# Kernel optimization log

Measured on AMD Instinct MI355X. Metric: run time of the kernel, lower is better.

The kernel has to match this reference:

```python
import jax, jax.numpy as jnp
import numpy as np

EPS = 1e-5  # torch BatchNorm default eps
SLOPE = 0.2  # LeakyReLU negative slope


def bn_apply(h, p):
    # p: (4, C) stacked [gamma, beta, running_mean, running_var]; h channel-last
    g, b, m, v = p[0], p[1], p[2], p[3]
    return (h - m) * (g * jax.lax.rsqrt(v + EPS)) + b


def graph_feature(x, k):
    # x: (B, N, C) -> (B, N, k, 2C) = concat(neighbor - center, center)
    inner = jnp.einsum('bnc,bmc->bnm', x, x)
    sq = jnp.sum(x * x, axis=-1)
    # negative squared pairwise distance (B, N, N)
    pd = 2.0 * inner - sq[:, :, None] - sq[:, None, :]
    idx = jax.lax.top_k(pd, k)[1]  # (B, N, k)
    nbr = jax.vmap(lambda xb, ib: xb[ib])(x, idx)  # (B, N, k, C) gather
    ctr = jnp.broadcast_to(x[:, :, None, :], nbr.shape)
    return jnp.concatenate([nbr - ctr, ctr], axis=-1)


def edge_block(h, w, bnp, k):
    # h: (B, N, C); w: (O, 2C) 1x1 conv weight; returns (B, N, O) after max over k
    f = graph_feature(h, k)
    z = jnp.einsum('bnkc,oc->bnko', f, w)
    z = jax.nn.leaky_relu(bn_apply(z, bnp), SLOPE)
    return jnp.max(z, axis=2)


def setup_inputs() -> dict:
    key = jax.random.key(0)
    ks = jax.random.split(key, 10)
    B, N, K = 16, 1024, 20
    emb, ncls = 1024, 40

    def bnp(c):
        return jnp.stack([jnp.ones(c), jnp.zeros(c), jnp.zeros(c), jnp.ones(c)])

    s = 0.05
    return {
        'x': jax.random.normal(ks[0], (B, 3, N), dtype=jnp.float32),
        'w1': jax.random.normal(ks[1], (64, 6), dtype=jnp.float32) * s,
        'bn1': bnp(64),
        'w2': jax.random.normal(ks[2], (64, 128), dtype=jnp.float32) * s,
        'bn2': bnp(64),
        'w3': jax.random.normal(ks[3], (128, 128), dtype=jnp.float32) * s,
        'bn3': bnp(128),
        'w4': jax.random.normal(ks[4], (256, 256), dtype=jnp.float32) * s,
        'bn4': bnp(256),
        'w5': jax.random.normal(ks[5], (emb, 512), dtype=jnp.float32) * s,
        'bn5': bnp(emb),
        'wl1': jax.random.normal(ks[6], (512, 2 * emb), dtype=jnp.float32) * s,
        'bn6': bnp(512),
        'wl2': jax.random.normal(ks[7], (256, 512), dtype=jnp.float32) * s,
        'bn7': bnp(256),
        'wl3': jax.random.normal(ks[8], (ncls, 256), dtype=jnp.float32) * s,
        'bl3': jax.random.normal(ks[9], (ncls,), dtype=jnp.float32) * s,
        'k': K,
    }


def reference(x, w1, bn1, w2, bn2, w3, bn3, w4, bn4, w5, bn5,
              wl1, bn6, wl2, bn7, wl3, bl3, k):
    # x: (B, 3, N) -> logits (B, num_classes); eval-mode BN, dropout = identity
    h0 = jnp.transpose(x, (0, 2, 1))  # (B, N, 3)
    x1 = edge_block(h0, w1, bn1, k)   # (B, N, 64)
    x2 = edge_block(x1, w2, bn2, k)   # (B, N, 64)
    x3 = edge_block(x2, w3, bn3, k)   # (B, N, 128)
    x4 = edge_block(x3, w4, bn4, k)   # (B, N, 256)
    h = jnp.concatenate([x1, x2, x3, x4], axis=-1)  # (B, N, 512)
    h = jax.nn.leaky_relu(bn_apply(jnp.einsum('bnc,oc->bno', h, w5), bn5), SLOPE)
    p = jnp.concatenate([jnp.max(h, axis=1), jnp.mean(h, axis=1)], axis=-1)  # (B, 2*emb)
    h = jax.nn.leaky_relu(bn_apply(p @ wl1.T, bn6), SLOPE)
    h = jax.nn.leaky_relu(bn_apply(h @ wl2.T, bn7), SLOPE)
    return h @ wl3.T + bl3
```

## Files before the change

### kernel.cpp

```cpp
#include <hip/hip_runtime.h>

#define BB 16
#define NN 1024
#define KNN 20
#define BNEPS 1e-5f

typedef __attribute__((ext_vector_type(8))) short short8;
typedef __attribute__((ext_vector_type(4))) float f32x4;

__device__ __forceinline__ float4 ld4(const float* p){ return *(const float4*)p; }
__device__ __forceinline__ void fma4(float4& a, float s, float4 w){
  a.x = fmaf(s, w.x, a.x); a.y = fmaf(s, w.y, a.y);
  a.z = fmaf(s, w.z, a.z); a.w = fmaf(s, w.w, a.w);
}
__device__ __forceinline__ void max4(float4& a, float4 v){
  a.x = fmaxf(a.x, v.x); a.y = fmaxf(a.y, v.y);
  a.z = fmaxf(a.z, v.z); a.w = fmaxf(a.w, v.w);
}
__device__ __forceinline__ unsigned short f2bf(float f){
  unsigned int u = __float_as_uint(f);
  u = (u + 0x7FFF + ((u >> 16) & 1)) >> 16;
  return (unsigned short)u;
}
__device__ __forceinline__ float bf2f(unsigned short u){
  return __uint_as_float(((unsigned int)u) << 16);
}
__device__ __forceinline__ f32x4 mfma16(short8 a, short8 b, f32x4 c){
  return __builtin_amdgcn_mfma_f32_16x16x32_bf16(a, b, c, 0, 0, 0);
}

__device__ __forceinline__ void top3_build(const float* rp, int kmr,
                                           float& a0, float& a1, float& a2,
                                           int& i0, int& i1, int& i2){
  a0 = -1e30f; a1 = -1e30f; a2 = -1e30f; i0 = 0; i1 = 0; i2 = 0;
#pragma unroll
  for (int r = 0; r < 4; r++){
    float4 t = ld4(rp + r*4);
    float tv[4] = {t.x, t.y, t.z, t.w};
#pragma unroll
    for (int q = 0; q < 4; q++){
      int e = r*4 + q;
      float v = ((kmr >> e) & 1) ? -1e30f : tv[q];
      bool b0 = v > a0, b1 = v > a1, b2 = v > a2;
      a2 = b1 ? a1 : (b2 ? v : a2); i2 = b1 ? i1 : (b2 ? e : i2);
      a1 = b0 ? a0 : (b1 ? v : a1); i1 = b0 ? i0 : (b1 ? e : i1);
      a0 = b0 ? v  : a0;            i0 = b0 ? e : i0;
    }
  }
}

__global__ __launch_bounds__(256) void k_transpose(const float* __restrict__ x, float* __restrict__ xt,
                                                   unsigned short* __restrict__ hlo,
                                                   float* __restrict__ sq){
  int i = blockIdx.x*256 + threadIdx.x;
  if (i >= BB*NN) return;
  int b = i >> 10, n = i & 1023;
  const float* xb = x + (size_t)b*3*NN;
  float4 v;
  v.x = xb[0*NN+n]; v.y = xb[1*NN+n]; v.z = xb[2*NN+n]; v.w = 0.f;
  ((float4*)xt)[i] = v;
  unsigned short hx = f2bf(v.x), hy = f2bf(v.y), hz = f2bf(v.z);
  float rx = v.x - bf2f(hx), ry = v.y - bf2f(hy), rz = v.z - bf2f(hz);
  unsigned short lx = f2bf(rx), ly = f2bf(ry), lz = f2bf(rz);
  float ex = bf2f(hx)+bf2f(lx), ey = bf2f(hy)+bf2f(ly), ez = bf2f(hz)+bf2f(lz);
  sq[i] = ex*ex + ey*ey + ez*ez;
  ushort4 h4 = {hx, hy, hz, 0};
  ushort4 l4 = {lx, ly, lz, 0};
  ushort4 z4 = {0, 0, 0, 0};
  unsigned short* pa = hlo + (size_t)i*512 + 256;
  unsigned short* pb = hlo + (size_t)i*512 + 288;
  *(ushort4*)(pa+0) = h4; *(ushort4*)(pa+4) = l4; *(ushort4*)(pa+8) = h4;
  *(ushort4*)(pb+0) = h4; *(ushort4*)(pb+4) = h4; *(ushort4*)(pb+8) = l4;
#pragma unroll
  for (int s = 12; s < 32; s += 4){ *(ushort4*)(pa+s) = z4; *(ushort4*)(pb+s) = z4; }
}

__device__ __forceinline__ void prep_w_dev(int i, const float* w, const float* bnp,
                                           float* wlT, float* dT, float* bias, int Cin, int Cpad, int Cout){
  if (i >= Cpad*Cout) return;
  int c = i / Cout, o = i - c*Cout;
  float s = bnp[o] * rsqrtf(bnp[3*Cout+o] + BNEPS);
  float wl = (c < Cin) ? w[(size_t)o*2*Cin + c] : 0.f;
  float wr = (c < Cin) ? w[(size_t)o*2*Cin + Cin + c] : 0.f;
  wlT[i] = wl * s;
  dT[i]  = (wr - wl) * s;
  if (c == 0) bias[o] = bnp[Cout+o] - bnp[2*Cout+o]*s;
}
__device__ __forceinline__ void prep_wbf_dev(int i, const float* w, const float* bnp,
                                             unsigned short* wlB, unsigned short* dB, float* bias,
                                             int Cin, int Cout){
  if (i >= Cin*Cout) return;
  int o = i / Cin, c = i - o*Cin;
  float s = bnp[o] * rsqrtf(bnp[3*Cout+o] + BNEPS);
  float wl = w[(size_t)o*2*Cin + c] * s;
  float wr = w[(size_t)o*2*Cin + Cin + c] * s;
  wlB[i] = f2bf(wl);
  dB[i]  = f2bf(wr - wl);
  if (c == 0) bias[o] = bnp[Cout+o] - bnp[2*Cout+o]*s;
}

__global__ __launch_bounds__(256) void k_prep_all(const float* __restrict__ w1, const float* __restrict__ bn1,
                                                  const float* __restrict__ w2, const float* __restrict__ bn2,
                                                  const float* __restrict__ w3, const float* __restrict__ bn3,
                                                  const float* __restrict__ w4, const float* __restrict__ bn4,
                                                  const float* __restrict__ w5, const float* __restrict__ bn5,
                                                  float* __restrict__ wlT1, float* __restrict__ dT1, float* __restrict__ bias1,
                                                  unsigned short* __restrict__ wlB2, unsigned short* __restrict__ dB2, float* __restrict__ bias2,
                                                  unsigned short* __restrict__ wlB3, unsigned short* __restrict__ dB3, float* __restrict__ bias3,
                                                  unsigned short* __restrict__ wlB4, unsigned short* __restrict__ dB4, float* __restrict__ bias4,
                                                  unsigned short* __restrict__ w5b, float* __restrict__ b5){
  int bid = blockIdx.x, t = threadIdx.x;
  if (bid < 1){
    prep_w_dev(t, w1, bn1, wlT1, dT1, bias1, 3, 4, 64);
  } else if (bid < 17){
    prep_wbf_dev((bid-1)*256 + t, w2, bn2, wlB2, dB2, bias2, 64, 64);
  } else if (bid < 49){
    prep_wbf_dev((bid-17)*256 + t, w3, bn3, wlB3, dB3, bias3, 64, 128);
  } else if (bid < 177){
    prep_wbf_dev((bid-49)*256 + t, w4, bn4, wlB4, dB4, bias4, 128, 256);
  } else {
    int i = (bid-177)*256 + t;
    int o = i >> 9, c = i & 511;
    float s = bn5[o] * rsqrtf(bn5[3*1024+o] + BNEPS);
    w5b[i] = f2bf(w5[(size_t)o*512 + c] * s);
    if (c == 0) b5[o] = bn5[1024+o] - bn5[2*1024+o]*s;
  }
}

template<int CC>
__global__ __launch_bounds__(256) void k_pdm(const unsigned short* __restrict__ hbi,
                                             const unsigned short* __restrict__ hlo,
                                             const float* __restrict__ sq,
                                             float* __restrict__ pd){
  __shared__ char sm[20480];
  char* As = sm; char* Bs = sm + 10240;
  const int tid = threadIdx.x, lane = tid & 63, w = tid >> 6;
  const int l15 = lane & 15, quad = lane >> 4;
  const int bid = blockIdx.x;
  const int xcd = bid & 7, j = bid >> 3;
  const int b = xcd + ((j >> 6) << 3);
  const int rt = (j >> 3) & 7, ct = j & 7;
  const size_t ar0 = (size_t)b*NN + rt*128;
  const size_t br0 = (size_t)b*NN + ct*128;
  const int colb = ct*128;

  f32x4 acc[2][8];
  f32x4 zero = {0.f,0.f,0.f,0.f};
#pragma unroll
  for (int i = 0; i < 2; i++)
#pragma unroll
    for (int j2 = 0; j2 < 8; j2++) acc[i][j2] = zero;

  for (int k0 = 0; k0 < 3*CC; k0 += 32){
    int seg = k0 / CC, off = k0 - seg*CC;
    const unsigned short* Ap = (seg == 1) ? hlo : hbi;
    const unsigned short* Bp = (seg == 2) ? hlo : hbi;
#pragma unroll
    for (int i = 0; i < 2; i++){
      int e = tid + i*256;
      int r = e >> 2, sg = e & 3;
      *(float4*)(As + r*80 + sg*16) = *(const float4*)(Ap + (ar0+r)*512 + off + sg*8);
      *(float4*)(Bs + r*80 + sg*16) = *(const float4*)(Bp + (br0+r)*512 + off + sg*8);
    }
    __syncthreads();
    short8 af0 = *(short8*)(As + (w*32 + l15)*80 + quad*16);
    short8 af1 = *(short8*)(As + (w*32 + 16 + l15)*80 + quad*16);
#pragma unroll
    for (int ns = 0; ns < 8; ns++){
      short8 bf = *(short8*)(Bs + (ns*16 + l15)*80 + quad*16);
      acc[0][ns] = mfma16(af0, bf, acc[0][ns]);
      acc[1][ns] = mfma16(af1, bf, acc[1][ns]);
    }
    __syncthreads();
  }

  float* L = (float*)sm;
#pragma unroll
  for (int p = 0; p < 4; p++){
    const int ms = p >> 1, nh = p & 1;
    __syncthreads();
#pragma unroll
    for (int ns = 0; ns < 4; ns++){
      f32x4 a = acc[ms][nh*4 + ns];
      float sqv = sq[br0 + (nh*4+ns)*16 + l15];
#pragma unroll
      for (int r = 0; r < 4; r++)
        L[(w*16 + quad*4 + r)*68 + ns*16 + l15] = 2.f*a[r] - sqv;
    }
    __syncthreads();
#pragma unroll
    for (int k = 0; k < 4; k++){
      int e = tid + k*256;
      int lr = e >> 4, c4 = (e & 15)*4;
      int grow = (int)ar0 + (lr >> 4)*32 + ms*16 + (lr & 15);
      *(float4*)(pd + (size_t)grow*NN + colb + nh*64 + c4) = *(float4*)(L + lr*68 + c4);
    }
  }
}

__global__ __launch_bounds__(256) void k_pdm1(const unsigned short* __restrict__ hlo,
                                              const float* __restrict__ sq,
                                              float* __restrict__ pd){
  __shared__ char sm[20480];
  char* As = sm; char* Bs = sm + 10240;
  const int tid = threadIdx.x, lane = tid & 63, w = tid >> 6;
  const int l15 = lane & 15, quad = lane >> 4;
  const int bid = blockIdx.x;
  const int xcd = bid & 7, j = bid >> 3;
  const int b = xcd + ((j >> 6) << 3);
  const int rt = (j >> 3) & 7, ct = j & 7;
  const size_t ar0 = (size_t)b*NN + rt*128;
  const size_t br0 = (size_t)b*NN + ct*128;
  const int colb = ct*128;

#pragma unroll
  for (int i = 0; i < 2; i++){
    int e = tid + i*256;
    int r = e >> 2, sg = e & 3;
    *(float4*)(As + r*80 + sg*16) = *(const float4*)(hlo + (ar0+r)*512 + 256 + sg*8);
    *(float4*)(Bs + r*80 + sg*16) = *(const float4*)(hlo + (br0+r)*512 + 288 + sg*8);
  }
  __syncthreads();

  f32x4 acc[2][8];
  f32x4 zero = {0.f,0.f,0.f,0.f};
#pragma unroll
  for (int i = 0; i < 2; i++)
#pragma unroll
    for (int j2 = 0; j2 < 8; j2++) acc[i][j2] = zero;

  short8 af0 = *(short8*)(As + (w*32 + l15)*80 + quad*16);
  short8 af1 = *(short8*)(As + (w*32 + 16 + l15)*80 + quad*16);
#pragma unroll
  for (int ns = 0; ns < 8; ns++){
    short8 bf = *(short8*)(Bs + (ns*16 + l15)*80 + quad*16);
    acc[0][ns] = mfma16(af0, bf, acc[0][ns]);
    acc[1][ns] = mfma16(af1, bf, acc[1][ns]);
  }

  float* L = (float*)sm;
#pragma unroll
  for (int p = 0; p < 4; p++){
    const int ms = p >> 1, nh = p & 1;
    __syncthreads();
#pragma unroll
    for (int ns = 0; ns < 4; ns++){
      f32x4 a = acc[ms][nh*4 + ns];
      float sqv = sq[br0 + (nh*4+ns)*16 + l15];
#pragma unroll
      for (int r = 0; r < 4; r++)
        L[(w*16 + quad*4 + r)*68 + ns*16 + l15] = 2.f*a[r] - sqv;
    }
    __syncthreads();
#pragma unroll
    for (int k = 0; k < 4; k++){
      int e = tid + k*256;
      int lr = e >> 4, c4 = (e & 15)*4;
      int grow = (int)ar0 + (lr >> 4)*32 + ms*16 + (lr & 15);
      *(float4*)(pd + (size_t)grow*NN + colb + nh*64 + c4) = *(float4*)(L + lr*68 + c4);
    }
  }
}

__global__ __launch_bounds__(256) void k_topk(const float* __restrict__ pd, int* __restrict__ idxOut){
  int w = threadIdx.x >> 6, lane = threadIdx.x & 63;
  const int bid = blockIdx.x;
  const int xcd = bid & 7, j = bid >> 3;
  const int b = xcd + ((j >> 7) << 3);
  const int local = j & 127;
  int bn0 = (b*128 + local)*8 + w*2;
  const float* row0 = pd + (size_t)bn0*NN + lane*16;
  const float* row1 = row0 + NN;

  float c0v[2], c1v[2], c2v[2];
  int   c0i[2], c1i[2], c2i[2];
  int   km[2] = {0, 0};
  top3_build(row0, 0, c0v[0], c1v[0], c2v[0], c0i[0], c1i[0], c2i[0]);
  top3_build(row1, 0, c0v[1], c1v[1], c2v[1], c0i[1], c1i[1], c2i[1]);

  int* out0 = idxOut + (size_t)bn0*KNN;
  int* out1 = out0 + KNN;
  for (int it = 0; it < KNN; it++){
    float g0 = c0v[0], g1 = c0v[1];
#pragma unroll
    for (int s = 1; s < 64; s <<= 1){
      g0 = fmaxf(g0, __shfl_xor(g0, s));
      g1 = fmaxf(g1, __shfl_xor(g1, s));
    }
    int o0 = __ffsll(__ballot(c0v[0] == g0)) - 1;
    int o1 = __ffsll(__ballot(c0v[1] == g1)) - 1;
    bool u0 = (lane == o0), u1 = (lane == o1);
    if (u0) out0[it] = lane*16 + c0i[0];
    if (u1) out1[it] = lane*16 + c0i[1];
    km[0] |= u0 ? (1 << c0i[0]) : 0;
    km[1] |= u1 ? (1 << c0i[1]) : 0;
    c0v[0] = u0 ? c1v[0] : c0v[0];  c0i[0] = u0 ? c1i[0] : c0i[0];
    c1v[0] = u0 ? c2v[0] : c1v[0];  c1i[0] = u0 ? c2i[0] : c1i[0];
    c2v[0] = u0 ? -1e30f : c2v[0];
    c0v[1] = u1 ? c1v[1] : c0v[1];  c0i[1] = u1 ? c1i[1] : c0i[1];
    c1v[1] = u1 ? c2v[1] : c1v[1];  c1i[1] = u1 ? c2i[1] : c1i[1];
    c2v[1] = u1 ? -1e30f : c2v[1];
    if (it < KNN-1){
      bool rp0 = (c0v[0] == -1e30f) && (km[0] != 0xFFFF);
      bool rp1 = (c0v[1] == -1e30f) && (km[1] != 0xFFFF);
      if (__ballot(rp0 || rp1)){
        if (rp0) top3_build(row0, km[0], c0v[0], c1v[0], c2v[0], c0i[0], c1i[0], c2i[0]);
        if (rp1) top3_build(row1, km[1], c0v[1], c1v[1], c2v[1], c0i[1], c1i[1], c2i[1]);
      }
    }
  }
}

__global__ __launch_bounds__(256) void k_uv1(const float* __restrict__ xt,
                                             const float* __restrict__ wlT, const float* __restrict__ dT,
                                             float* __restrict__ Z){
  const int bid = blockIdx.x;
  const int pb = ((bid >> 10) << 10) | ((bid & 7) << 7) | ((bid >> 3) & 127);
  int t = pb*256 + threadIdx.x;
  int n = t >> 5, q = t & 31;
  float4 xv = ld4(xt + (size_t)n*4);
  const float* wp = (q < 16) ? (wlT + q*4) : (dT + (q-16)*4);
  float4 a = make_float4(0.f,0.f,0.f,0.f);
  fma4(a, xv.x, ld4(wp + 0*64));
  fma4(a, xv.y, ld4(wp + 1*64));
  fma4(a, xv.z, ld4(wp + 2*64));
  fma4(a, xv.w, ld4(wp + 3*64));
  *(float4*)(Z + (size_t)n*128 + q*4) = a;
}

template<int K>
__global__ __launch_bounds__(256) void k_uv(const unsigned short* __restrict__ hbi,
                                            const unsigned short* __restrict__ wB,
                                            float* __restrict__ Z, int ldz){
  __shared__ char sm[20480];
  char* As = sm; char* Bs = sm + 10240;
  const int tid = threadIdx.x, lane = tid & 63, w = tid >> 6;
  const int l15 = lane & 15, quad = lane >> 4;
  const int bx = blockIdx.x;
  const int t = ((bx & 7) << 3) | ((bx >> 3) & 7) | (bx & 64);
  const int n0 = blockIdx.y*128, r0 = t*128;

  f32x4 acc[2][8];
  f32x4 zero = {0.f,0.f,0.f,0.f};
#pragma unroll
  for (int i = 0; i < 2; i++)
#pragma unroll
    for (int j = 0; j < 8; j++) acc[i][j] = zero;

  for (int k0 = 0; k0 < K; k0 += 32){
#pragma unroll
    for (int i = 0; i < 2; i++){
      int e = tid + i*256;
      int r = e >> 2, sg = e & 3;
      *(float4*)(As + r*80 + sg*16) = *(const float4*)(hbi + ((size_t)(r0+r))*512 + k0 + sg*8);
      *(float4*)(Bs + r*80 + sg*16) = *(const float4*)(wB  + ((size_t)(n0+r))*K   + k0 + sg*8);
    }
    __syncthreads();
    short8 af0 = *(short8*)(As + (w*32 + l15)*80 + quad*16);
    short8 af1 = *(short8*)(As + (w*32 + 16 + l15)*80 + quad*16);
#pragma unroll
    for (int ns = 0; ns < 8; ns++){
      short8 bf = *(short8*)(Bs + (ns*16 + l15)*80 + quad*16);
      acc[0][ns] = mfma16(af0, bf, acc[0][ns]);
      acc[1][ns] = mfma16(af1, bf, acc[1][ns]);
    }
    __syncthreads();
  }

#pragma unroll
  for (int ms = 0; ms < 2; ms++){
#pragma unroll
    for (int ns = 0; ns < 8; ns++){
      f32x4 a = acc[ms][ns];
      int row = r0 + w*32 + ms*16 + quad*4;
      int col = n0 + ns*16 + l15;
#pragma unroll
      for (int r = 0; r < 4; r++)
        Z[(size_t)(row+r)*ldz + col] = a[r];
    }
  }
}

template<int COUT, int P, bool WLO>
__global__ __launch_bounds__(256) void k_gmax(const float* __restrict__ Z,
                                              const float* __restrict__ bias,
                                              const int* __restrict__ knn_idx,
                                              unsigned short* __restrict__ hbo,
                                              unsigned short* __restrict__ hloo,
                                              float* __restrict__ sqo){
  constexpr int QPP = COUT/4;
  constexpr int BPB = 1024/P;
  constexpr int SHF = (P == 16) ? 6 : (P == 8) ? 7 : 8;
  __shared__ int idxS[P*KNN];
  const int tid = threadIdx.x;
  const int bid = blockIdx.x;
  const int pb = ((bid >> (SHF+3)) << (SHF+3)) | ((bid & 7) << SHF) | ((bid >> 3) & (BPB-1));
  const int p0 = pb * P;
  for (int t = tid; t < P*KNN; t += 256) idxS[t] = knn_idx[(size_t)p0*KNN + t];
  __syncthreads();

  const int p = tid / QPP, q = tid - p*QPP;
  const int base = p0 & ~1023;
  const int ldz = 2*COUT;
  const float* Zq = Z + q*4;

  float4 m = make_float4(-1e30f,-1e30f,-1e30f,-1e30f);
#pragma unroll
  for (int j = 0; j < KNN; j++){
    int mr = idxS[p*KNN + j];
    max4(m, ld4(Zq + (size_t)(base + mr)*ldz));
  }
  float4 ctr = ld4(Z + (size_t)(p0+p)*ldz + COUT + q*4);
  float4 bs  = ld4(bias + q*4);
  float4 y;
  y.x = m.x + ctr.x + bs.x; y.x = fmaxf(y.x, 0.2f*y.x);
  y.y = m.y + ctr.y + bs.y; y.y = fmaxf(y.y, 0.2f*y.y);
  y.z = m.z + ctr.z + bs.z; y.z = fmaxf(y.z, 0.2f*y.z);
  y.w = m.w + ctr.w + bs.w; y.w = fmaxf(y.w, 0.2f*y.w);

  size_t pi = (size_t)(p0 + p);
  ushort4 hv; hv.x = f2bf(y.x); hv.y = f2bf(y.y); hv.z = f2bf(y.z); hv.w = f2bf(y.w);
  *(ushort4*)(hbo + pi*512 + q*4) = hv;
  if (WLO){
    ushort4 lv;
    lv.x = f2bf(y.x - bf2f(hv.x)); lv.y = f2bf(y.y - bf2f(hv.y));
    lv.z = f2bf(y.z - bf2f(hv.z)); lv.w = f2bf(y.w - bf2f(hv.w));
    *(ushort4*)(hloo + pi*512 + q*4) = lv;
    float ex = bf2f(hv.x)+bf2f(lv.x), ey = bf2f(hv.y)+bf2f(lv.y);
    float ez = bf2f(hv.z)+bf2f(lv.z), ew = bf2f(hv.w)+bf2f(lv.w);
    float s4 = ex*ex + ey*ey + ez*ez + ew*ew;
#pragma unroll
    for (int sh = 1; sh < QPP; sh <<= 1) s4 += __shfl_xor(s4, sh);
    if (q == 0) sqo[pi] = s4;
  }
}

__global__ __launch_bounds__(256) void k_conv5m(const unsigned short* __restrict__ hb,
                                                const unsigned short* __restrict__ w5b,
                                                const float* __restrict__ b5,
                                                float* __restrict__ pmax, float* __restrict__ psum){
  __shared__ char sm[20480 + 4096];
  char* As = sm; char* Bs = sm + 10240;
  float* red = (float*)(sm + 20480);
  const int tid = threadIdx.x, lane = tid & 63, w = tid >> 6;
  const int l15 = lane & 15, quad = lane >> 4;
  const int n0 = blockIdx.y*128, r0 = blockIdx.x*128;

  f32x4 acc[2][8];
  f32x4 zero = {0.f,0.f,0.f,0.f};
#pragma unroll
  for (int i = 0; i < 2; i++)
#pragma unroll
    for (int j = 0; j < 8; j++) acc[i][j] = zero;

  for (int k0 = 0; k0 < 512; k0 += 32){
#pragma unroll
    for (int i = 0; i < 2; i++){
      int e = tid + i*256;
      int r = e >> 2, sg = e & 3;
      *(float4*)(As + r*80 + sg*16) = *(const float4*)(hb  + ((size_t)(r0+r))*512 + k0 + sg*8);
      *(float4*)(Bs + r*80 + sg*16) = *(const float4*)(w5b + ((size_t)(n0+r))*512 + k0 + sg*8);
    }
    __syncthreads();
    short8 af0 = *(short8*)(As + (w*32 + l15)*80 + quad*16);
    short8 af1 = *(short8*)(As + (w*32 + 16 + l15)*80 + quad*16);
#pragma unroll
    for (int ns = 0; ns < 8; ns++){
      short8 bf = *(short8*)(Bs + (ns*16 + l15)*80 + quad*16);
      acc[0][ns] = mfma16(af0, bf, acc[0][ns]);
      acc[1][ns] = mfma16(af1, bf, acc[1][ns]);
    }
    __syncthreads();
  }

#pragma unroll
  for (int ns = 0; ns < 8; ns++){
    float bv = b5[n0 + ns*16 + l15];
    float mx = -1e30f, sum = 0.f;
#pragma unroll
    for (int ms = 0; ms < 2; ms++){
      float* a = (float*)&acc[ms][ns];
#pragma unroll
      for (int r = 0; r < 4; r++){
        float v = a[r] + bv; v = fmaxf(v, 0.2f*v);
        mx = fmaxf(mx, v); sum += v;
      }
    }
    for (int s = 16; s < 64; s <<= 1){
      mx = fmaxf(mx, __shfl_xor(mx, s));
      sum += __shfl_xor(sum, s);
    }
    if (quad == 0){ red[(w*8 + ns)*16 + l15] = mx; red[512 + (w*8 + ns)*16 + l15] = sum; }
  }
  __syncthreads();
  if (tid < 128){
    int ns = tid >> 4, ci = tid & 15;
    float mx = -1e30f, sum = 0.f;
#pragma unroll
    for (int w2 = 0; w2 < 4; w2++){
      mx = fmaxf(mx, red[(w2*8 + ns)*16 + ci]);
      sum += red[512 + (w2*8 + ns)*16 + ci];
    }
    pmax[(size_t)blockIdx.x*1024 + n0 + tid] = mx;
    psum[(size_t)blockIdx.x*1024 + n0 + tid] = sum;
  }
}

__global__ __launch_bounds__(256) void k_fc1(const float* __restrict__ pmax, const float* __restrict__ psum,
                                             const float* __restrict__ wl1, const float* __restrict__ bn6,
                                             float* __restrict__ h1){
  __shared__ float pS[2048];
  const int b = blockIdx.y, t = threadIdx.x;
  for (int f = t; f < 512; f += 256){
    float4 r;
    if (f < 256){
      r = ld4(pmax + (size_t)(b*8)*1024 + f*4);
#pragma unroll
      for (int ch = 1; ch < 8; ch++) max4(r, ld4(pmax + (size_t)(b*8+ch)*1024 + f*4));
    } else {
      int o = (f-256)*4;
      r = ld4(psum + (size_t)(b*8)*1024 + o);
#pragma unroll
      for (int ch = 1; ch < 8; ch++){
        float4 s = ld4(psum + (size_t)(b*8+ch)*1024 + o);
        r.x += s.x; r.y += s.y; r.z += s.z; r.w += s.w;
      }
      r.x *= (1.f/1024.f); r.y *= (1.f/1024.f); r.z *= (1.f/1024.f); r.w *= (1.f/1024.f);
    }
    ((float4*)pS)[f] = r;
  }
  __syncthreads();
  const int ol = t >> 4, ch = t & 15;
  const int o = blockIdx.x*16 + ol;
  const float* wr = wl1 + (size_t)o*2048;
  float acc = 0.f;
#pragma unroll
  for (int j = 0; j < 32; j++){
    int c = ch*4 + j*64;
    float4 wv = ld4(wr + c);
    acc += pS[c]*wv.x + pS[c+1]*wv.y + pS[c+2]*wv.z + pS[c+3]*wv.w;
  }
#pragma unroll
  for (int s = 1; s < 16; s <<= 1) acc += __shfl_xor(acc, s);
  if (ch == 0){
    float s = bn6[o] * rsqrtf(bn6[3*512+o] + BNEPS);
    float y = (acc - bn6[2*512+o])*s + bn6[512+o];
    h1[(size_t)b*512 + o] = fmaxf(y, 0.2f*y);
  }
}

__global__ __launch_bounds__(256) void k_fc2(const float* __restrict__ h1,
                                             const float* __restrict__ wl2, const float* __restrict__ bn7,
                                             float* __restrict__ h2){
  __shared__ float hS[512];
  const int b = blockIdx.y, t = threadIdx.x;
  if (t < 128) ((float4*)hS)[t] = ((const float4*)(h1 + (size_t)b*512))[t];
  __syncthreads();
  const int ol = t >> 4, ch = t & 15;
  const int o = blockIdx.x*16 + ol;
  const float* wr = wl2 + (size_t)o*512;
  float acc = 0.f;
#pragma unroll
  for (int j = 0; j < 8; j++){
    int c = ch*4 + j*64;
    float4 wv = ld4(wr + c);
    acc += hS[c]*wv.x + hS[c+1]*wv.y + hS[c+2]*wv.z + hS[c+3]*wv.w;
  }
#pragma unroll
  for (int s = 1; s < 16; s <<= 1) acc += __shfl_xor(acc, s);
  if (ch == 0){
    float s = bn7[o] * rsqrtf(bn7[3*256+o] + BNEPS);
    float y = (acc - bn7[2*256+o])*s + bn7[256+o];
    h2[(size_t)b*256 + o] = fmaxf(y, 0.2f*y);
  }
}

__global__ __launch_bounds__(64) void k_fc3(const float* __restrict__ h2,
                                            const float* __restrict__ wl3, const float* __restrict__ bl3,
                                            float* __restrict__ out){
  const int o = blockIdx.x, b = blockIdx.y, lane = threadIdx.x;
  float4 wv = ld4(wl3 + (size_t)o*256 + lane*4);
  float4 hv = ld4(h2 + (size_t)b*256 + lane*4);
  float acc = hv.x*wv.x + hv.y*wv.y + hv.z*wv.z + hv.w*wv.w;
#pragma unroll
  for (int s = 1; s < 64; s <<= 1) acc += __shfl_xor(acc, s);
  if (lane == 0) out[(size_t)b*40 + o] = acc + bl3[o];
}

extern "C" void kernel_launch(void* const* d_in, const int* in_sizes, int n_in,
                              void* d_out, int out_size, void* d_ws, size_t ws_size,
                              hipStream_t stream) {
  (void)in_sizes; (void)n_in; (void)out_size; (void)ws_size;
  const float* x   = (const float*)d_in[0];
  const float* w1  = (const float*)d_in[1];
  const float* bn1 = (const float*)d_in[2];
  const float* w2  = (const float*)d_in[3];
  const float* bn2 = (const float*)d_in[4];
  const float* w3  = (const float*)d_in[5];
  const float* bn3 = (const float*)d_in[6];
  const float* w4  = (const float*)d_in[7];
  const float* bn4 = (const float*)d_in[8];
  const float* w5  = (const float*)d_in[9];
  const float* bn5 = (const float*)d_in[10];
  const float* wl1 = (const float*)d_in[11];
  const float* bn6 = (const float*)d_in[12];
  const float* wl2 = (const float*)d_in[13];
  const float* bn7 = (const float*)d_in[14];
  const float* wl3 = (const float*)d_in[15];
  const float* bl3 = (const float*)d_in[16];
  float* out = (float*)d_out;

  float* ws    = (float*)d_ws;
  float* xt    = ws;
  float* sqb   = xt + 65536;
  int*   idxb  = (int*)(sqb + 16384);
  float* pd    = (float*)(idxb + 327680);
  unsigned short* hlo = (unsigned short*)(pd + 16777216);
  float* wlT1  = (float*)(hlo + 8388608);
  float* dT1   = wlT1 + 256;
  float* bias1 = dT1 + 256;
  float* bias2 = bias1 + 64;
  float* bias3 = bias2 + 64;
  float* bias4 = bias3 + 128;
  float* b5    = bias4 + 256;
  float* pmax  = b5 + 1024;
  float* psum  = pmax + 131072;
  float* pool  = psum + 131072;
  float* h1b   = pool + 32768;
  float* h2b   = h1b + 8192;
  unsigned short* hb   = (unsigned short*)(h2b + 4096);
  unsigned short* wlB2 = hb + (size_t)16384*512;
  unsigned short* dB2  = wlB2 + 4096;
  unsigned short* wlB3 = dB2 + 4096;
  unsigned short* dB3  = wlB3 + 8192;
  unsigned short* wlB4 = dB3 + 8192;
  unsigned short* dB4  = wlB4 + 32768;
  unsigned short* w5b  = dB4 + 32768;
  float* Z = pd;

  k_transpose<<<64, 256, 0, stream>>>(x, xt, hlo, sqb);
  k_prep_all<<<2225, 256, 0, stream>>>(w1, bn1, w2, bn2, w3, bn3, w4, bn4, w5, bn5,
                                       wlT1, dT1, bias1, wlB2, dB2, bias2,
                                       wlB3, dB3, bias3, wlB4, dB4, bias4, w5b, b5);

  k_pdm1<<<1024, 256, 0, stream>>>(hlo, sqb, pd);
  k_topk<<<2048, 256, 0, stream>>>(pd, idxb);
  k_uv1<<<2048, 256, 0, stream>>>(xt, wlT1, dT1, Z);
  k_gmax<64,16,true><<<1024, 256, 0, stream>>>(Z, bias1, idxb, hb, hlo, sqb);

  k_pdm<64><<<1024, 256, 0, stream>>>(hb, hlo, sqb, pd);
  k_topk<<<2048, 256, 0, stream>>>(pd, idxb);
  k_uv<64><<<dim3(128,1), 256, 0, stream>>>(hb, wlB2, Z, 128);
  k_gmax<64,16,true><<<1024, 256, 0, stream>>>(Z, bias2, idxb, hb + 64, hlo + 64, sqb);

  k_pdm<64><<<1024, 256, 0, stream>>>(hb + 64, hlo + 64, sqb, pd);
  k_topk<<<2048, 256, 0, stream>>>(pd, idxb);
  k_uv<64><<<dim3(128,2), 256, 0, stream>>>(hb + 64, wlB3, Z, 256);
  k_gmax<128,8,true><<<2048, 256, 0, stream>>>(Z, bias3, idxb, hb + 128, hlo + 128, sqb);

  k_pdm<128><<<1024, 256, 0, stream>>>(hb + 128, hlo + 128, sqb, pd);
  k_topk<<<2048, 256, 0, stream>>>(pd, idxb);
  k_uv<128><<<dim3(128,4), 256, 0, stream>>>(hb + 128, wlB4, Z, 512);
  k_gmax<256,4,false><<<4096, 256, 0, stream>>>(Z, bias4, idxb, hb + 256, nullptr, nullptr);

  k_conv5m<<<dim3(128,8), 256, 0, stream>>>(hb, w5b, b5, pmax, psum);
  k_fc1<<<dim3(32,16), 256, 0, stream>>>(pmax, psum, wl1, bn6, h1b);
  k_fc2<<<dim3(16,16), 256, 0, stream>>>(h1b, wl2, bn7, h2b);
  k_fc3<<<dim3(40,16), 64, 0, stream>>>(h2b, wl3, bl3, out);
}
```

Before: 422.1 us.

## Co-launch top-k with per-point projection GEMM and merge init kernels

Runs top-k selection and the per-point weight projection GEMM in one launch, with blocks split by index range. Z gets its own buffer, so the two no longer alias pd and can run concurrently. The transpose and weight-prep kernels are also merged into one init launch. This cuts launch overhead and lets independent work overlap to fill the GPU, at the cost of a larger workspace and mixed block types sharing occupancy.

```diff
diff --git a/kernel.cpp b/kernel.cpp
--- a/kernel.cpp
+++ b/kernel.cpp
@@ -49,222 +49,9 @@
   }
 }
 
-__global__ __launch_bounds__(256) void k_transpose(const float* __restrict__ x, float* __restrict__ xt,
-                                                   unsigned short* __restrict__ hlo,
-                                                   float* __restrict__ sq){
-  int i = blockIdx.x*256 + threadIdx.x;
-  if (i >= BB*NN) return;
-  int b = i >> 10, n = i & 1023;
-  const float* xb = x + (size_t)b*3*NN;
-  float4 v;
-  v.x = xb[0*NN+n]; v.y = xb[1*NN+n]; v.z = xb[2*NN+n]; v.w = 0.f;
-  ((float4*)xt)[i] = v;
-  unsigned short hx = f2bf(v.x), hy = f2bf(v.y), hz = f2bf(v.z);
-  float rx = v.x - bf2f(hx), ry = v.y - bf2f(hy), rz = v.z - bf2f(hz);
-  unsigned short lx = f2bf(rx), ly = f2bf(ry), lz = f2bf(rz);
-  float ex = bf2f(hx)+bf2f(lx), ey = bf2f(hy)+bf2f(ly), ez = bf2f(hz)+bf2f(lz);
-  sq[i] = ex*ex + ey*ey + ez*ez;
-  ushort4 h4 = {hx, hy, hz, 0};
-  ushort4 l4 = {lx, ly, lz, 0};
-  ushort4 z4 = {0, 0, 0, 0};
-  unsigned short* pa = hlo + (size_t)i*512 + 256;
-  unsigned short* pb = hlo + (size_t)i*512 + 288;
-  *(ushort4*)(pa+0) = h4; *(ushort4*)(pa+4) = l4; *(ushort4*)(pa+8) = h4;
-  *(ushort4*)(pb+0) = h4; *(ushort4*)(pb+4) = h4; *(ushort4*)(pb+8) = l4;
-#pragma unroll
-  for (int s = 12; s < 32; s += 4){ *(ushort4*)(pa+s) = z4; *(ushort4*)(pb+s) = z4; }
-}
-
-__device__ __forceinline__ void prep_w_dev(int i, const float* w, const float* bnp,
-                                           float* wlT, float* dT, float* bias, int Cin, int Cpad, int Cout){
-  if (i >= Cpad*Cout) return;
-  int c = i / Cout, o = i - c*Cout;
-  float s = bnp[o] * rsqrtf(bnp[3*Cout+o] + BNEPS);
-  float wl = (c < Cin) ? w[(size_t)o*2*Cin + c] : 0.f;
-  float wr = (c < Cin) ? w[(size_t)o*2*Cin + Cin + c] : 0.f;
-  wlT[i] = wl * s;
-  dT[i]  = (wr - wl) * s;
-  if (c == 0) bias[o] = bnp[Cout+o] - bnp[2*Cout+o]*s;
-}
-__device__ __forceinline__ void prep_wbf_dev(int i, const float* w, const float* bnp,
-                                             unsigned short* wlB, unsigned short* dB, float* bias,
-                                             int Cin, int Cout){
-  if (i >= Cin*Cout) return;
-  int o = i / Cin, c = i - o*Cin;
-  float s = bnp[o] * rsqrtf(bnp[3*Cout+o] + BNEPS);
-  float wl = w[(size_t)o*2*Cin + c] * s;
-  float wr = w[(size_t)o*2*Cin + Cin + c] * s;
-  wlB[i] = f2bf(wl);
-  dB[i]  = f2bf(wr - wl);
-  if (c == 0) bias[o] = bnp[Cout+o] - bnp[2*Cout+o]*s;
-}
-
-__global__ __launch_bounds__(256) void k_prep_all(const float* __restrict__ w1, const float* __restrict__ bn1,
-                                                  const float* __restrict__ w2, const float* __restrict__ bn2,
-                                                  const float* __restrict__ w3, const float* __restrict__ bn3,
-                                                  const float* __restrict__ w4, const float* __restrict__ bn4,
-                                                  const float* __restrict__ w5, const float* __restrict__ bn5,
-                                                  float* __restrict__ wlT1, float* __restrict__ dT1, float* __restrict__ bias1,
-                                                  unsigned short* __restrict__ wlB2, unsigned short* __restrict__ dB2, float* __restrict__ bias2,
-                                                  unsigned short* __restrict__ wlB3, unsigned short* __restrict__ dB3, float* __restrict__ bias3,
-                                                  unsigned short* __restrict__ wlB4, unsigned short* __restrict__ dB4, float* __restrict__ bias4,
-                                                  unsigned short* __restrict__ w5b, float* __restrict__ b5){
-  int bid = blockIdx.x, t = threadIdx.x;
-  if (bid < 1){
-    prep_w_dev(t, w1, bn1, wlT1, dT1, bias1, 3, 4, 64);
-  } else if (bid < 17){
-    prep_wbf_dev((bid-1)*256 + t, w2, bn2, wlB2, dB2, bias2, 64, 64);
-  } else if (bid < 49){
-    prep_wbf_dev((bid-17)*256 + t, w3, bn3, wlB3, dB3, bias3, 64, 128);
-  } else if (bid < 177){
-    prep_wbf_dev((bid-49)*256 + t, w4, bn4, wlB4, dB4, bias4, 128, 256);
-  } else {
-    int i = (bid-177)*256 + t;
-    int o = i >> 9, c = i & 511;
-    float s = bn5[o] * rsqrtf(bn5[3*1024+o] + BNEPS);
-    w5b[i] = f2bf(w5[(size_t)o*512 + c] * s);
-    if (c == 0) b5[o] = bn5[1024+o] - bn5[2*1024+o]*s;
-  }
-}
-
-template<int CC>
-__global__ __launch_bounds__(256) void k_pdm(const unsigned short* __restrict__ hbi,
-                                             const unsigned short* __restrict__ hlo,
-                                             const float* __restrict__ sq,
-                                             float* __restrict__ pd){
-  __shared__ char sm[20480];
-  char* As = sm; char* Bs = sm + 10240;
-  const int tid = threadIdx.x, lane = tid & 63, w = tid >> 6;
-  const int l15 = lane & 15, quad = lane >> 4;
-  const int bid = blockIdx.x;
-  const int xcd = bid & 7, j = bid >> 3;
-  const int b = xcd + ((j >> 6) << 3);
-  const int rt = (j >> 3) & 7, ct = j & 7;
-  const size_t ar0 = (size_t)b*NN + rt*128;
-  const size_t br0 = (size_t)b*NN + ct*128;
-  const int colb = ct*128;
-
-  f32x4 acc[2][8];
-  f32x4 zero = {0.f,0.f,0.f,0.f};
-#pragma unroll
-  for (int i = 0; i < 2; i++)
-#pragma unroll
-    for (int j2 = 0; j2 < 8; j2++) acc[i][j2] = zero;
-
-  for (int k0 = 0; k0 < 3*CC; k0 += 32){
-    int seg = k0 / CC, off = k0 - seg*CC;
-    const unsigned short* Ap = (seg == 1) ? hlo : hbi;
-    const unsigned short* Bp = (seg == 2) ? hlo : hbi;
-#pragma unroll
-    for (int i = 0; i < 2; i++){
-      int e = tid + i*256;
-      int r = e >> 2, sg = e & 3;
-      *(float4*)(As + r*80 + sg*16) = *(const float4*)(Ap + (ar0+r)*512 + off + sg*8);
-      *(float4*)(Bs + r*80 + sg*16) = *(const float4*)(Bp + (br0+r)*512 + off + sg*8);
-    }
-    __syncthreads();
-    short8 af0 = *(short8*)(As + (w*32 + l15)*80 + quad*16);
-    short8 af1 = *(short8*)(As + (w*32 + 16 + l15)*80 + quad*16);
-#pragma unroll
-    for (int ns = 0; ns < 8; ns++){
-      short8 bf = *(short8*)(Bs + (ns*16 + l15)*80 + quad*16);
-      acc[0][ns] = mfma16(af0, bf, acc[0][ns]);
-      acc[1][ns] = mfma16(af1, bf, acc[1][ns]);
-    }
-    __syncthreads();
-  }
-
-  float* L = (float*)sm;
-#pragma unroll
-  for (int p = 0; p < 4; p++){
-    const int ms = p >> 1, nh = p & 1;
-    __syncthreads();
-#pragma unroll
-    for (int ns = 0; ns < 4; ns++){
-      f32x4 a = acc[ms][nh*4 + ns];
-      float sqv = sq[br0 + (nh*4+ns)*16 + l15];
-#pragma unroll
-      for (int r = 0; r < 4; r++)
-        L[(w*16 + quad*4 + r)*68 + ns*16 + l15] = 2.f*a[r] - sqv;
-    }
-    __syncthreads();
-#pragma unroll
-    for (int k = 0; k < 4; k++){
-      int e = tid + k*256;
-      int lr = e >> 4, c4 = (e & 15)*4;
-      int grow = (int)ar0 + (lr >> 4)*32 + ms*16 + (lr & 15);
-      *(float4*)(pd + (size_t)grow*NN + colb + nh*64 + c4) = *(float4*)(L + lr*68 + c4);
-    }
-  }
-}
-
-__global__ __launch_bounds__(256) void k_pdm1(const unsigned short* __restrict__ hlo,
-                                              const float* __restrict__ sq,
-                                              float* __restrict__ pd){
-  __shared__ char sm[20480];
-  char* As = sm; char* Bs = sm + 10240;
-  const int tid = threadIdx.x, lane = tid & 63, w = tid >> 6;
-  const int l15 = lane & 15, quad = lane >> 4;
-  const int bid = blockIdx.x;
-  const int xcd = bid & 7, j = bid >> 3;
-  const int b = xcd + ((j >> 6) << 3);
-  const int rt = (j >> 3) & 7, ct = j & 7;
-  const size_t ar0 = (size_t)b*NN + rt*128;
-  const size_t br0 = (size_t)b*NN + ct*128;
-  const int colb = ct*128;
-
-#pragma unroll
-  for (int i = 0; i < 2; i++){
-    int e = tid + i*256;
-    int r = e >> 2, sg = e & 3;
-    *(float4*)(As + r*80 + sg*16) = *(const float4*)(hlo + (ar0+r)*512 + 256 + sg*8);
-    *(float4*)(Bs + r*80 + sg*16) = *(const float4*)(hlo + (br0+r)*512 + 288 + sg*8);
-  }
-  __syncthreads();
-
-  f32x4 acc[2][8];
-  f32x4 zero = {0.f,0.f,0.f,0.f};
-#pragma unroll
-  for (int i = 0; i < 2; i++)
-#pragma unroll
-    for (int j2 = 0; j2 < 8; j2++) acc[i][j2] = zero;
-
-  short8 af0 = *(short8*)(As + (w*32 + l15)*80 + quad*16);
-  short8 af1 = *(short8*)(As + (w*32 + 16 + l15)*80 + quad*16);
-#pragma unroll
-  for (int ns = 0; ns < 8; ns++){
-    short8 bf = *(short8*)(Bs + (ns*16 + l15)*80 + quad*16);
-    acc[0][ns] = mfma16(af0, bf, acc[0][ns]);
-    acc[1][ns] = mfma16(af1, bf, acc[1][ns]);
-  }
-
-  float* L = (float*)sm;
-#pragma unroll
-  for (int p = 0; p < 4; p++){
-    const int ms = p >> 1, nh = p & 1;
-    __syncthreads();
-#pragma unroll
-    for (int ns = 0; ns < 4; ns++){
-      f32x4 a = acc[ms][nh*4 + ns];
-      float sqv = sq[br0 + (nh*4+ns)*16 + l15];
-#pragma unroll
-      for (int r = 0; r < 4; r++)
-        L[(w*16 + quad*4 + r)*68 + ns*16 + l15] = 2.f*a[r] - sqv;
-    }
-    __syncthreads();
-#pragma unroll
-    for (int k = 0; k < 4; k++){
-      int e = tid + k*256;
-      int lr = e >> 4, c4 = (e & 15)*4;
-      int grow = (int)ar0 + (lr >> 4)*32 + ms*16 + (lr & 15);
-      *(float4*)(pd + (size_t)grow*NN + colb + nh*64 + c4) = *(float4*)(L + lr*68 + c4);
-    }
-  }
-}
-
-__global__ __launch_bounds__(256) void k_topk(const float* __restrict__ pd, int* __restrict__ idxOut){
-  int w = threadIdx.x >> 6, lane = threadIdx.x & 63;
-  const int bid = blockIdx.x;
+__device__ __forceinline__ void topk_body(int bid, int tidx,
+                                          const float* __restrict__ pd, int* __restrict__ idxOut){
+  int w = tidx >> 6, lane = tidx & 63;
   const int xcd = bid & 7, j = bid >> 3;
   const int b = xcd + ((j >> 7) << 3);
   const int local = j & 127;
@@ -311,10 +98,287 @@
   }
 }
 
-__global__ __launch_bounds__(256) void k_uv1(const float* __restrict__ xt,
-                                             const float* __restrict__ wlT, const float* __restrict__ dT,
-                                             float* __restrict__ Z){
+__device__ __forceinline__ void prep_w_dev(int i, const float* w, const float* bnp,
+                                           float* wlT, float* dT, float* bias, int Cin, int Cpad, int Cout){
+  if (i >= Cpad*Cout) return;
+  int c = i / Cout, o = i - c*Cout;
+  float s = bnp[o] * rsqrtf(bnp[3*Cout+o] + BNEPS);
+  float wl = (c < Cin) ? w[(size_t)o*2*Cin + c] : 0.f;
+  float wr = (c < Cin) ? w[(size_t)o*2*Cin + Cin + c] : 0.f;
+  wlT[i] = wl * s;
+  dT[i]  = (wr - wl) * s;
+  if (c == 0) bias[o] = bnp[Cout+o] - bnp[2*Cout+o]*s;
+}
+__device__ __forceinline__ void prep_wbf_dev(int i, const float* w, const float* bnp,
+                                             unsigned short* wlB, unsigned short* dB, float* bias,
+                                             int Cin, int Cout){
+  if (i >= Cin*Cout) return;
+  int o = i / Cin, c = i - o*Cin;
+  float s = bnp[o] * rsqrtf(bnp[3*Cout+o] + BNEPS);
+  float wl = w[(size_t)o*2*Cin + c] * s;
+  float wr = w[(size_t)o*2*Cin + Cin + c] * s;
+  wlB[i] = f2bf(wl);
+  dB[i]  = f2bf(wr - wl);
+  if (c == 0) bias[o] = bnp[Cout+o] - bnp[2*Cout+o]*s;
+}
+
+__global__ __launch_bounds__(256) void k_init(const float* __restrict__ x, float* __restrict__ xt,
+                                              unsigned short* __restrict__ hlo, float* __restrict__ sq,
+                                              const float* __restrict__ w1, const float* __restrict__ bn1,
+                                              const float* __restrict__ w2, const float* __restrict__ bn2,
+                                              const float* __restrict__ w3, const float* __restrict__ bn3,
+                                              const float* __restrict__ w4, const float* __restrict__ bn4,
+                                              const float* __restrict__ w5, const float* __restrict__ bn5,
+                                              float* __restrict__ wlT1, float* __restrict__ dT1, float* __restrict__ bias1,
+                                              unsigned short* __restrict__ wlB2, unsigned short* __restrict__ dB2, float* __restrict__ bias2,
+                                              unsigned short* __restrict__ wlB3, unsigned short* __restrict__ dB3, float* __restrict__ bias3,
+                                              unsigned short* __restrict__ wlB4, unsigned short* __restrict__ dB4, float* __restrict__ bias4,
+                                              unsigned short* __restrict__ w5b, float* __restrict__ b5){
+  const int t = threadIdx.x;
+  if (blockIdx.x < 64){
+    int i = blockIdx.x*256 + t;
+    int b = i >> 10, n = i & 1023;
+    const float* xb = x + (size_t)b*3*NN;
+    float4 v;
+    v.x = xb[0*NN+n]; v.y = xb[1*NN+n]; v.z = xb[2*NN+n]; v.w = 0.f;
+    ((float4*)xt)[i] = v;
+    unsigned short hx = f2bf(v.x), hy = f2bf(v.y), hz = f2bf(v.z);
+    float rx = v.x - bf2f(hx), ry = v.y - bf2f(hy), rz = v.z - bf2f(hz);
+    unsigned short lx = f2bf(rx), ly = f2bf(ry), lz = f2bf(rz);
+    float ex = bf2f(hx)+bf2f(lx), ey = bf2f(hy)+bf2f(ly), ez = bf2f(hz)+bf2f(lz);
+    sq[i] = ex*ex + ey*ey + ez*ez;
+    ushort4 h4 = {hx, hy, hz, 0};
+    ushort4 l4 = {lx, ly, lz, 0};
+    ushort4 z4 = {0, 0, 0, 0};
+    unsigned short* pa = hlo + (size_t)i*512 + 256;
+    unsigned short* pb = hlo + (size_t)i*512 + 288;
+    *(ushort4*)(pa+0) = h4; *(ushort4*)(pa+4) = l4; *(ushort4*)(pa+8) = h4;
+    *(ushort4*)(pb+0) = h4; *(ushort4*)(pb+4) = h4; *(ushort4*)(pb+8) = l4;
+#pragma unroll
+    for (int s = 12; s < 32; s += 4){ *(ushort4*)(pa+s) = z4; *(ushort4*)(pb+s) = z4; }
+    return;
+  }
+  int bid = blockIdx.x - 64;
+  if (bid < 1){
+    prep_w_dev(t, w1, bn1, wlT1, dT1, bias1, 3, 4, 64);
+  } else if (bid < 17){
+    prep_wbf_dev((bid-1)*256 + t, w2, bn2, wlB2, dB2, bias2, 64, 64);
+  } else if (bid < 49){
+    prep_wbf_dev((bid-17)*256 + t, w3, bn3, wlB3, dB3, bias3, 64, 128);
+  } else if (bid < 177){
+    prep_wbf_dev((bid-49)*256 + t, w4, bn4, wlB4, dB4, bias4, 128, 256);
+  } else {
+    int i = (bid-177)*256 + t;
+    int o = i >> 9, c = i & 511;
+    float s = bn5[o] * rsqrtf(bn5[3*1024+o] + BNEPS);
+    w5b[i] = f2bf(w5[(size_t)o*512 + c] * s);
+    if (c == 0) b5[o] = bn5[1024+o] - bn5[2*1024+o]*s;
+  }
+}
+
+template<int CC>
+__global__ __launch_bounds__(256) void k_pdm(const unsigned short* __restrict__ hbi,
+                                             const unsigned short* __restrict__ hlo,
+                                             const float* __restrict__ sq,
+                                             float* __restrict__ pd){
+  __shared__ char sm[20480];
+  char* As = sm; char* Bs = sm + 10240;
+  const int tid = threadIdx.x, lane = tid & 63, w = tid >> 6;
+  const int l15 = lane & 15, quad = lane >> 4;
   const int bid = blockIdx.x;
+  const int xcd = bid & 7, j = bid >> 3;
+  const int b = xcd + ((j >> 6) << 3);
+  const int rt = (j >> 3) & 7, ct = j & 7;
+  const size_t ar0 = (size_t)b*NN + rt*128;
+  const size_t br0 = (size_t)b*NN + ct*128;
+  const int colb = ct*128;
+
+  f32x4 acc[2][8];
+  f32x4 zero = {0.f,0.f,0.f,0.f};
+#pragma unroll
+  for (int i = 0; i < 2; i++)
+#pragma unroll
+    for (int j2 = 0; j2 < 8; j2++) acc[i][j2] = zero;
+
+  for (int k0 = 0; k0 < 3*CC; k0 += 32){
+    int seg = k0 / CC, off = k0 - seg*CC;
+    const unsigned short* Ap = (seg == 1) ? hlo : hbi;
+    const unsigned short* Bp = (seg == 2) ? hlo : hbi;
+#pragma unroll
+    for (int i = 0; i < 2; i++){
+      int e = tid + i*256;
+      int r = e >> 2, sg = e & 3;
+      *(float4*)(As + r*80 + sg*16) = *(const float4*)(Ap + (ar0+r)*512 + off + sg*8);
+      *(float4*)(Bs + r*80 + sg*16) = *(const float4*)(Bp + (br0+r)*512 + off + sg*8);
+    }
+    __syncthreads();
+    short8 af0 = *(short8*)(As + (w*32 + l15)*80 + quad*16);
+    short8 af1 = *(short8*)(As + (w*32 + 16 + l15)*80 + quad*16);
+#pragma unroll
+    for (int ns = 0; ns < 8; ns++){
+      short8 bf = *(short8*)(Bs + (ns*16 + l15)*80 + quad*16);
+      acc[0][ns] = mfma16(af0, bf, acc[0][ns]);
+      acc[1][ns] = mfma16(af1, bf, acc[1][ns]);
+    }
+    __syncthreads();
+  }
+
+  float* L = (float*)sm;
+#pragma unroll
+  for (int p = 0; p < 4; p++){
+    const int ms = p >> 1, nh = p & 1;
+    __syncthreads();
+#pragma unroll
+    for (int ns = 0; ns < 4; ns++){
+      f32x4 a = acc[ms][nh*4 + ns];
+      float sqv = sq[br0 + (nh*4+ns)*16 + l15];
+#pragma unroll
+      for (int r = 0; r < 4; r++)
+        L[(w*16 + quad*4 + r)*68 + ns*16 + l15] = 2.f*a[r] - sqv;
+    }
+    __syncthreads();
+#pragma unroll
+    for (int k = 0; k < 4; k++){
+      int e = tid + k*256;
+      int lr = e >> 4, c4 = (e & 15)*4;
+      int grow = (int)ar0 + (lr >> 4)*32 + ms*16 + (lr & 15);
+      *(float4*)(pd + (size_t)grow*NN + colb + nh*64 + c4) = *(float4*)(L + lr*68 + c4);
+    }
+  }
+}
+
+__global__ __launch_bounds__(256) void k_pdm1(const unsigned short* __restrict__ hlo,
+                                              const float* __restrict__ sq,
+                                              float* __restrict__ pd){
+  __shared__ char sm[20480];
+  char* As = sm; char* Bs = sm + 10240;
+  const int tid = threadIdx.x, lane = tid & 63, w = tid >> 6;
+  const int l15 = lane & 15, quad = lane >> 4;
+  const int bid = blockIdx.x;
+  const int xcd = bid & 7, j = bid >> 3;
+  const int b = xcd + ((j >> 6) << 3);
+  const int rt = (j >> 3) & 7, ct = j & 7;
+  const size_t ar0 = (size_t)b*NN + rt*128;
+  const size_t br0 = (size_t)b*NN + ct*128;
+  const int colb = ct*128;
+
+#pragma unroll
+  for (int i = 0; i < 2; i++){
+    int e = tid + i*256;
+    int r = e >> 2, sg = e & 3;
+    *(float4*)(As + r*80 + sg*16) = *(const float4*)(hlo + (ar0+r)*512 + 256 + sg*8);
+    *(float4*)(Bs + r*80 + sg*16) = *(const float4*)(hlo + (br0+r)*512 + 288 + sg*8);
+  }
+  __syncthreads();
+
+  f32x4 acc[2][8];
+  f32x4 zero = {0.f,0.f,0.f,0.f};
+#pragma unroll
+  for (int i = 0; i < 2; i++)
+#pragma unroll
+    for (int j2 = 0; j2 < 8; j2++) acc[i][j2] = zero;
+
+  short8 af0 = *(short8*)(As + (w*32 + l15)*80 + quad*16);
+  short8 af1 = *(short8*)(As + (w*32 + 16 + l15)*80 + quad*16);
+#pragma unroll
+  for (int ns = 0; ns < 8; ns++){
+    short8 bf = *(short8*)(Bs + (ns*16 + l15)*80 + quad*16);
+    acc[0][ns] = mfma16(af0, bf, acc[0][ns]);
+    acc[1][ns] = mfma16(af1, bf, acc[1][ns]);
+  }
+
+  float* L = (float*)sm;
+#pragma unroll
+  for (int p = 0; p < 4; p++){
+    const int ms = p >> 1, nh = p & 1;
+    __syncthreads();
+#pragma unroll
+    for (int ns = 0; ns < 4; ns++){
+      f32x4 a = acc[ms][nh*4 + ns];
+      float sqv = sq[br0 + (nh*4+ns)*16 + l15];
+#pragma unroll
+      for (int r = 0; r < 4; r++)
+        L[(w*16 + quad*4 + r)*68 + ns*16 + l15] = 2.f*a[r] - sqv;
+    }
+    __syncthreads();
+#pragma unroll
+    for (int k = 0; k < 4; k++){
+      int e = tid + k*256;
+      int lr = e >> 4, c4 = (e & 15)*4;
+      int grow = (int)ar0 + (lr >> 4)*32 + ms*16 + (lr & 15);
+      *(float4*)(pd + (size_t)grow*NN + colb + nh*64 + c4) = *(float4*)(L + lr*68 + c4);
+    }
+  }
+}
+
+template<int K, int NY>
+__global__ __launch_bounds__(256) void k_tkuv(const float* __restrict__ pd, int* __restrict__ idxOut,
+                                              const unsigned short* __restrict__ hbi,
+                                              const unsigned short* __restrict__ wB,
+                                              float* __restrict__ Z, int ldz){
+  __shared__ char sm[20480];
+  if (blockIdx.x < 2048){
+    topk_body(blockIdx.x, threadIdx.x, pd, idxOut);
+    return;
+  }
+  char* As = sm; char* Bs = sm + 10240;
+  const int tid = threadIdx.x, lane = tid & 63, w = tid >> 6;
+  const int l15 = lane & 15, quad = lane >> 4;
+  const int jj = blockIdx.x - 2048;
+  const int bx = jj & 127;
+  const int t = ((bx & 7) << 3) | ((bx >> 3) & 7) | (bx & 64);
+  const int n0 = (jj >> 7)*128, r0 = t*128;
+
+  f32x4 acc[2][8];
+  f32x4 zero = {0.f,0.f,0.f,0.f};
+#pragma unroll
+  for (int i = 0; i < 2; i++)
+#pragma unroll
+    for (int j = 0; j < 8; j++) acc[i][j] = zero;
+
+  for (int k0 = 0; k0 < K; k0 += 32){
+#pragma unroll
+    for (int i = 0; i < 2; i++){
+      int e = tid + i*256;
+      int r = e >> 2, sg = e & 3;
+      *(float4*)(As + r*80 + sg*16) = *(const float4*)(hbi + ((size_t)(r0+r))*512 + k0 + sg*8);
+      *(float4*)(Bs + r*80 + sg*16) = *(const float4*)(wB  + ((size_t)(n0+r))*K   + k0 + sg*8);
+    }
+    __syncthreads();
+    short8 af0 = *(short8*)(As + (w*32 + l15)*80 + quad*16);
+    short8 af1 = *(short8*)(As + (w*32 + 16 + l15)*80 + quad*16);
+#pragma unroll
+    for (int ns = 0; ns < 8; ns++){
+      short8 bf = *(short8*)(Bs + (ns*16 + l15)*80 + quad*16);
+      acc[0][ns] = mfma16(af0, bf, acc[0][ns]);
+      acc[1][ns] = mfma16(af1, bf, acc[1][ns]);
+    }
+    __syncthreads();
+  }
+
+#pragma unroll
+  for (int ms = 0; ms < 2; ms++){
+#pragma unroll
+    for (int ns = 0; ns < 8; ns++){
+      f32x4 a = acc[ms][ns];
+      int row = r0 + w*32 + ms*16 + quad*4;
+      int col = n0 + ns*16 + l15;
+#pragma unroll
+      for (int r = 0; r < 4; r++)
+        Z[(size_t)(row+r)*ldz + col] = a[r];
+    }
+  }
+}
+
+__global__ __launch_bounds__(256) void k_tkuv1(const float* __restrict__ pd, int* __restrict__ idxOut,
+                                               const float* __restrict__ xt,
+                                               const float* __restrict__ wlT, const float* __restrict__ dT,
+                                               float* __restrict__ Z){
+  if (blockIdx.x < 2048){
+    topk_body(blockIdx.x, threadIdx.x, pd, idxOut);
+    return;
+  }
+  const int bid = blockIdx.x - 2048;
   const int pb = ((bid >> 10) << 10) | ((bid & 7) << 7) | ((bid >> 3) & 127);
   int t = pb*256 + threadIdx.x;
   int n = t >> 5, q = t & 31;
@@ -326,59 +390,6 @@
   fma4(a, xv.z, ld4(wp + 2*64));
   fma4(a, xv.w, ld4(wp + 3*64));
   *(float4*)(Z + (size_t)n*128 + q*4) = a;
-}
-
-template<int K>
-__global__ __launch_bounds__(256) void k_uv(const unsigned short* __restrict__ hbi,
-                                            const unsigned short* __restrict__ wB,
-                                            float* __restrict__ Z, int ldz){
-  __shared__ char sm[20480];
-  char* As = sm; char* Bs = sm + 10240;
-  const int tid = threadIdx.x, lane = tid & 63, w = tid >> 6;
-  const int l15 = lane & 15, quad = lane >> 4;
-  const int bx = blockIdx.x;
-  const int t = ((bx & 7) << 3) | ((bx >> 3) & 7) | (bx & 64);
-  const int n0 = blockIdx.y*128, r0 = t*128;
-
-  f32x4 acc[2][8];
-  f32x4 zero = {0.f,0.f,0.f,0.f};
-#pragma unroll
-  for (int i = 0; i < 2; i++)
-#pragma unroll
-    for (int j = 0; j < 8; j++) acc[i][j] = zero;
-
-  for (int k0 = 0; k0 < K; k0 += 32){
-#pragma unroll
-    for (int i = 0; i < 2; i++){
-      int e = tid + i*256;
-      int r = e >> 2, sg = e & 3;
-      *(float4*)(As + r*80 + sg*16) = *(const float4*)(hbi + ((size_t)(r0+r))*512 + k0 + sg*8);
-      *(float4*)(Bs + r*80 + sg*16) = *(const float4*)(wB  + ((size_t)(n0+r))*K   + k0 + sg*8);
-    }
-    __syncthreads();
-    short8 af0 = *(short8*)(As + (w*32 + l15)*80 + quad*16);
-    short8 af1 = *(short8*)(As + (w*32 + 16 + l15)*80 + quad*16);
-#pragma unroll
-    for (int ns = 0; ns < 8; ns++){
-      short8 bf = *(short8*)(Bs + (ns*16 + l15)*80 + quad*16);
-      acc[0][ns] = mfma16(af0, bf, acc[0][ns]);
-      acc[1][ns] = mfma16(af1, bf, acc[1][ns]);
-    }
-    __syncthreads();
-  }
-
-#pragma unroll
-  for (int ms = 0; ms < 2; ms++){
-#pragma unroll
-    for (int ns = 0; ns < 8; ns++){
-      f32x4 a = acc[ms][ns];
-      int row = r0 + w*32 + ms*16 + quad*4;
-      int col = n0 + ns*16 + l15;
-#pragma unroll
-      for (int r = 0; r < 4; r++)
-        Z[(size_t)(row+r)*ldz + col] = a[r];
-    }
-  }
 }
 
 template<int COUT, int P, bool WLO>
@@ -636,31 +647,27 @@
   unsigned short* wlB4 = dB3 + 8192;
   unsigned short* dB4  = wlB4 + 32768;
   unsigned short* w5b  = dB4 + 32768;
-  float* Z = pd;
-
-  k_transpose<<<64, 256, 0, stream>>>(x, xt, hlo, sqb);
-  k_prep_all<<<2225, 256, 0, stream>>>(w1, bn1, w2, bn2, w3, bn3, w4, bn4, w5, bn5,
-                                       wlT1, dT1, bias1, wlB2, dB2, bias2,
-                                       wlB3, dB3, bias3, wlB4, dB4, bias4, w5b, b5);
+  float* Z = (float*)(w5b + 524288);
+
+  k_init<<<2289, 256, 0, stream>>>(x, xt, hlo, sqb,
+                                   w1, bn1, w2, bn2, w3, bn3, w4, bn4, w5, bn5,
+                                   wlT1, dT1, bias1, wlB2, dB2, bias2,
+                                   wlB3, dB3, bias3, wlB4, dB4, bias4, w5b, b5);
 
   k_pdm1<<<1024, 256, 0, stream>>>(hlo, sqb, pd);
-  k_topk<<<2048, 256, 0, stream>>>(pd, idxb);
-  k_uv1<<<2048, 256, 0, stream>>>(xt, wlT1, dT1, Z);
+  k_tkuv1<<<4096, 256, 0, stream>>>(pd, idxb, xt, wlT1, dT1, Z);
   k_gmax<64,16,true><<<1024, 256, 0, stream>>>(Z, bias1, idxb, hb, hlo, sqb);
 
   k_pdm<64><<<1024, 256, 0, stream>>>(hb, hlo, sqb, pd);
-  k_topk<<<2048, 256, 0, stream>>>(pd, idxb);
-  k_uv<64><<<dim3(128,1), 256, 0, stream>>>(hb, wlB2, Z, 128);
+  k_tkuv<64,1><<<2048+128, 256, 0, stream>>>(pd, idxb, hb, wlB2, Z, 128);
   k_gmax<64,16,true><<<1024, 256, 0, stream>>>(Z, bias2, idxb, hb + 64, hlo + 64, sqb);
 
   k_pdm<64><<<1024, 256, 0, stream>>>(hb + 64, hlo + 64, sqb, pd);
-  k_topk<<<2048, 256, 0, stream>>>(pd, idxb);
-  k_uv<64><<<dim3(128,2), 256, 0, stream>>>(hb + 64, wlB3, Z, 256);
+  k_tkuv<64,2><<<2048+256, 256, 0, stream>>>(pd, idxb, hb + 64, wlB3, Z, 256);
   k_gmax<128,8,true><<<2048, 256, 0, stream>>>(Z, bias3, idxb, hb + 128, hlo + 128, sqb);
 
   k_pdm<128><<<1024, 256, 0, stream>>>(hb + 128, hlo + 128, sqb, pd);
-  k_topk<<<2048, 256, 0, stream>>>(pd, idxb);
-  k_uv<128><<<dim3(128,4), 256, 0, stream>>>(hb + 128, wlB4, Z, 512);
+  k_tkuv<128,4><<<2048+512, 256, 0, stream>>>(pd, idxb, hb + 128, wlB4, Z, 512);
   k_gmax<256,4,false><<<4096, 256, 0, stream>>>(Z, bias4, idxb, hb + 256, nullptr, nullptr);
 
   k_conv5m<<<dim3(128,8), 256, 0, stream>>>(hb, w5b, b5, pmax, psum);
```

New measurement: 403.4 us (median of 2 runs). -4.4%, faster.
